# Kernel tuning notes

Hardware: AMD Instinct MI355X
Metric: run time of the kernel (lower is better)

Reference implementation:

```python
import jax, jax.numpy as jnp
import numpy as np
import math

BATCH = 8192
INPUT_DIM = 4096
N_FEATURES = 2048
HAD = 4096  # 2**ceil(log2(max(input_dim, n_features)))
SCALE = math.sqrt(2.0 / N_FEATURES)
INV_SQRT_HAD = 1.0 / math.sqrt(HAD)


def fwht(x):
    """Fast Walsh-Hadamard transform, exact replica of the torch butterfly.
    x: [B, HAD] -> [B, HAD], scaled by 1/sqrt(HAD)."""
    B = x.shape[0]
    h = 1
    while h < HAD:  # log2(HAD) iterations, fixed at trace time
        x = x.reshape(B, -1, h, 2)
        x = jnp.concatenate([x[..., 0] + x[..., 1], x[..., 0] - x[..., 1]], axis=-1)
        x = x.reshape(B, -1)
        h *= 2
    return x * INV_SQRT_HAD


def setup_inputs() -> dict:
    key = jax.random.key(0)
    kx, k1, k2, k3, kp, kb = jax.random.split(key, 6)
    x = jax.random.normal(kx, (BATCH, INPUT_DIM), dtype=jnp.float32)
    D1 = jnp.sign(jax.random.normal(k1, (HAD,), dtype=jnp.float32))
    D2 = jnp.sign(jax.random.normal(k2, (HAD,), dtype=jnp.float32))
    D3 = jnp.sign(jax.random.normal(k3, (HAD,), dtype=jnp.float32))
    perm = jax.random.permutation(kp, HAD)
    bias = jax.random.uniform(kb, (N_FEATURES,), dtype=jnp.float32) * (2.0 * math.pi)
    return {"x": x, "D1": D1, "D2": D2, "D3": D3, "bias": bias, "perm": perm}


def reference(x, D1, D2, D3, bias, perm):
    # pad to hadamard_dim if needed (no-op here since INPUT_DIM == HAD)
    if x.shape[1] < HAD:
        x = jnp.pad(x, ((0, 0), (0, HAD - x.shape[1])))
    x = x * D1
    x = fwht(x)
    x = x * D2
    x = fwht(x)
    x = x * D3
    x = x[:, perm]          # random permutation of columns
    x = x[:, :N_FEATURES]   # keep first n_features columns
    return SCALE * jnp.cos(x + bias)
```

## Files before the change

### kernel.cpp

```cpp
#include <hip/hip_runtime.h>

#define HADN 4096
#define NFEAT 2048
#define INV2PI 0.15915494309189535f

typedef float floatx4 __attribute__((ext_vector_type(4)));
typedef const __attribute__((address_space(1))) void* gas_cptr;
typedef __attribute__((address_space(3))) void* las_ptr;

__device__ __forceinline__ void gload_lds16(const float* g, float* l) {
  __builtin_amdgcn_global_load_lds(
      (gas_cptr)(unsigned long long)g,
      (las_ptr)(unsigned)(unsigned long long)l, 16, 0, 0);
}

__device__ __host__ __forceinline__ int pi_map(int q) {
  return  (((q >> 3) & 1))
        | (((q >> 11) & 1) << 1)
        | (((q >> 7) & 1) << 2)
        | (((q >> 1) & 1) << 3)
        | (((q >> 5) & 1) << 4)
        | (((q >> 9) & 1) << 5)
        | (((q >> 0) & 1) << 6)
        | (((q >> 2) & 1) << 7)
        | (((q >> 4) & 1) << 8)
        | (((q >> 6) & 1) << 9)
        | (((q >> 8) & 1) << 10)
        | (((q >> 10) & 1) << 11);
}

__device__ __host__ __forceinline__ int pi_inv_map(int p) {
  return  (((p >> 6) & 1))
        | (((p >> 3) & 1) << 1)
        | (((p >> 7) & 1) << 2)
        | (((p >> 0) & 1) << 3)
        | (((p >> 8) & 1) << 4)
        | (((p >> 4) & 1) << 5)
        | (((p >> 9) & 1) << 6)
        | (((p >> 2) & 1) << 7)
        | (((p >> 10) & 1) << 8)
        | (((p >> 5) & 1) << 9)
        | (((p >> 11) & 1) << 10)
        | (((p >> 1) & 1) << 11);
}

__device__ __forceinline__ int swz(int p) {
  return p ^ ((((p >> 6) ^ (p >> 9)) & 7) << 2);
}

template <int BIT>
__device__ __forceinline__ void bfly(float* r) {
#pragma unroll
  for (int e = 0; e < 16; ++e) {
    if ((e & BIT) == 0) {
      const int f = e | BIT;
      const float a = r[e], b = r[f];
      r[e] = a + b;
      r[f] = a - b;
    }
  }
}

template <int CTRL>
__device__ __forceinline__ void dpp_bfly(float* r, bool upper) {
  const unsigned sm = upper ? 0x80000000u : 0u;
#pragma unroll
  for (int e = 0; e < 16; ++e) {
    const int pv = __builtin_amdgcn_update_dpp(
        0, __float_as_int(r[e]), CTRL, 0xF, 0xF, true);
    r[e] = __int_as_float(pv) + __int_as_float(__float_as_int(r[e]) ^ sm);
  }
}

__global__ __launch_bounds__(256) void srf_setup(
    const float* __restrict__ D1, const float* __restrict__ D2,
    const float* __restrict__ D3, const int* __restrict__ perm,
    const float* __restrict__ bias,
    unsigned* __restrict__ D1sgn, unsigned* __restrict__ D2sgn,
    float* __restrict__ dgc, int* __restrict__ gidx,
    float* __restrict__ bzc) {
  const int i = blockIdx.x * 256 + threadIdx.x;
  const bool b1 = (__float_as_uint(D1[i]) >> 31) != 0;
  const bool b2 = (__float_as_uint(D2[pi_inv_map(i)]) >> 31) != 0;
  const unsigned long long m1 = __ballot(b1);
  const unsigned long long m2 = __ballot(b2);
  const int lane = i & 63;
  if ((lane & 31) == 0) {
    D1sgn[i >> 5] = (unsigned)(m1 >> (lane & 32));
    D2sgn[i >> 5] = (unsigned)(m2 >> (lane & 32));
  }
  if (i < NFEAT) {
    const int j = perm[i];
    gidx[i] = swz(pi_map(pi_map(j)));
    dgc[i] = 0.0625f * INV2PI * D3[j];
    bzc[i] = INV2PI * bias[i];
  }
}

__global__ __launch_bounds__(512) void srf_main(
    const float* __restrict__ x,
    const unsigned* __restrict__ D1sgn, const unsigned* __restrict__ D2sgn,
    const float* __restrict__ dgc, const int* __restrict__ gidx,
    const float* __restrict__ bzc, float* __restrict__ out) {
  __shared__ float lds[2][HADN];
  const int tid = threadIdx.x;
  const int rr = tid >> 8;
  const int t256 = tid & 255;
  const long row = (long)blockIdx.x * 2;
  const int l = tid & 63;
  const int w = (tid >> 6) & 3;
  const int base = (((l >> 2) & 1) << 2) | ((l & 1) << 5) | (((l >> 3) & 1) << 6)
                 | (((l >> 4) & 1) << 7) | (((l >> 1) & 1) << 8)
                 | (((l >> 5) & 1) << 9) | (w << 10);

  const float* xr = x + (row + rr) * HADN;
#pragma unroll
  for (int k = 0; k < 4; ++k) {
    const int p = (k * 256 + t256) * 4;
    gload_lds16(xr + swz(p), &lds[rr][p]);
  }

  const unsigned sw1 = D1sgn[base >> 5] >> (base & 4);
  const unsigned sw2 = D2sgn[base >> 5] >> (base & 4);
  const int o = tid * 4;
  const int4   gi = *(const int4*)(gidx + o);
  const float4 dg = *(const float4*)(dgc + o);
  const float4 bz = *(const float4*)(bzc + o);
  __syncthreads();

  float r[16];
  float* L = &lds[rr][0];
#pragma unroll
  for (int g = 0; g < 4; ++g) {
    const int p = base | ((g & 1) << 3) | (((g >> 1) & 1) << 4);
    const float4 v = *(const float4*)(L + swz(p));
    r[g * 4 + 0] = v.x; r[g * 4 + 1] = v.y; r[g * 4 + 2] = v.z; r[g * 4 + 3] = v.w;
  }
#pragma unroll
  for (int e = 0; e < 16; ++e) {
    const int pos = (e & 3) | ((e & 12) << 1);
    r[e] = __int_as_float(__float_as_int(r[e]) ^ ((sw1 >> pos) << 31));
  }
  bfly<2>(r); bfly<4>(r); bfly<8>(r);
  dpp_bfly<0xB1>(r, (l & 1) != 0);
#pragma unroll
  for (int e = 0; e < 16; ++e) {
    const int pos = (e & 3) | ((e & 12) << 1);
    r[e] = __int_as_float(__float_as_int(r[e]) ^ ((sw2 >> pos) << 31));
  }
  bfly<1>(r); bfly<4>(r); bfly<8>(r);
  dpp_bfly<0x4E>(r, (l & 2) != 0);

#pragma unroll
  for (int g = 0; g < 4; ++g) {
    const int p = base | ((g & 1) << 3) | (((g >> 1) & 1) << 4);
    const float4 v = make_float4(r[g * 4 + 0], r[g * 4 + 1], r[g * 4 + 2], r[g * 4 + 3]);
    *(float4*)(L + swz(p)) = v;
  }
  __syncthreads();

  float* op = out + row * NFEAT;
  floatx4 res0;
  res0.x = 0.03125f * __builtin_amdgcn_cosf(fmaf(lds[0][gi.x], dg.x, bz.x));
  res0.y = 0.03125f * __builtin_amdgcn_cosf(fmaf(lds[0][gi.y], dg.y, bz.y));
  res0.z = 0.03125f * __builtin_amdgcn_cosf(fmaf(lds[0][gi.z], dg.z, bz.z));
  res0.w = 0.03125f * __builtin_amdgcn_cosf(fmaf(lds[0][gi.w], dg.w, bz.w));
  __builtin_nontemporal_store(res0, (floatx4*)(op + o));
  floatx4 res1;
  res1.x = 0.03125f * __builtin_amdgcn_cosf(fmaf(lds[1][gi.x], dg.x, bz.x));
  res1.y = 0.03125f * __builtin_amdgcn_cosf(fmaf(lds[1][gi.y], dg.y, bz.y));
  res1.z = 0.03125f * __builtin_amdgcn_cosf(fmaf(lds[1][gi.z], dg.z, bz.z));
  res1.w = 0.03125f * __builtin_amdgcn_cosf(fmaf(lds[1][gi.w], dg.w, bz.w));
  __builtin_nontemporal_store(res1, (floatx4*)(op + NFEAT + o));
}

extern "C" void kernel_launch(void* const* d_in, const int* in_sizes, int n_in,
                              void* d_out, int out_size, void* d_ws, size_t ws_size,
                              hipStream_t stream) {
  const float* x    = (const float*)d_in[0];
  const float* D1   = (const float*)d_in[1];
  const float* D2   = (const float*)d_in[2];
  const float* D3   = (const float*)d_in[3];
  const float* bias = (const float*)d_in[4];
  const int*   perm = (const int*)d_in[5];
  float* out = (float*)d_out;

  unsigned* D1sgn = (unsigned*)d_ws;
  unsigned* D2sgn = D1sgn + 128;
  float*    dgc   = (float*)(D2sgn + 128);
  int*      gidx  = (int*)(dgc + NFEAT);
  float*    bzc   = (float*)(gidx + NFEAT);

  srf_setup<<<16, 256, 0, stream>>>(D1, D2, D3, perm, bias,
                                    D1sgn, D2sgn, dgc, gidx, bzc);
  srf_main<<<4096, 512, 0, stream>>>(x, D1sgn, D2sgn, dgc, gidx, bzc, out);
}
```

Baseline: 40.01 us.

## Fuse setup into main kernel and process multiple row pairs per block

Removes the separate setup kernel. Each block now builds the D1/D2 sign bitmasks in LDS and computes the gather indices and scales itself. Each block also loops over four row pairs, which amortises that setup and cuts the grid to 1024 blocks. The next rows are loaded only after the current outputs are written, with no overlap between the two. That leaves the loop serialised, and fewer blocks can reduce latency hiding.

Result: slower. 44.66 us (+11.6%).

```diff
diff --git a/kernel.cpp b/kernel.cpp
--- a/kernel.cpp
+++ b/kernel.cpp
@@ -2,6 +2,8 @@
 
 #define HADN 4096
 #define NFEAT 2048
+#define ROWS_PER_IT 2
+#define ITERS 4
 #define INV2PI 0.15915494309189535f
 
 typedef float floatx4 __attribute__((ext_vector_type(4)));
@@ -14,7 +16,7 @@
       (las_ptr)(unsigned)(unsigned long long)l, 16, 0, 0);
 }
 
-__device__ __host__ __forceinline__ int pi_map(int q) {
+__device__ __forceinline__ int pi_map(int q) {
   return  (((q >> 3) & 1))
         | (((q >> 11) & 1) << 1)
         | (((q >> 7) & 1) << 2)
@@ -29,7 +31,7 @@
         | (((q >> 10) & 1) << 11);
 }
 
-__device__ __host__ __forceinline__ int pi_inv_map(int p) {
+__device__ __forceinline__ int pi_inv_map(int p) {
   return  (((p >> 6) & 1))
         | (((p >> 3) & 1) << 1)
         | (((p >> 7) & 1) << 2)
@@ -72,106 +74,122 @@
   }
 }
 
-__global__ __launch_bounds__(256) void srf_setup(
-    const float* __restrict__ D1, const float* __restrict__ D2,
-    const float* __restrict__ D3, const int* __restrict__ perm,
-    const float* __restrict__ bias,
-    unsigned* __restrict__ D1sgn, unsigned* __restrict__ D2sgn,
-    float* __restrict__ dgc, int* __restrict__ gidx,
-    float* __restrict__ bzc) {
-  const int i = blockIdx.x * 256 + threadIdx.x;
-  const bool b1 = (__float_as_uint(D1[i]) >> 31) != 0;
-  const bool b2 = (__float_as_uint(D2[pi_inv_map(i)]) >> 31) != 0;
-  const unsigned long long m1 = __ballot(b1);
-  const unsigned long long m2 = __ballot(b2);
-  const int lane = i & 63;
-  if ((lane & 31) == 0) {
-    D1sgn[i >> 5] = (unsigned)(m1 >> (lane & 32));
-    D2sgn[i >> 5] = (unsigned)(m2 >> (lane & 32));
-  }
-  if (i < NFEAT) {
-    const int j = perm[i];
-    gidx[i] = swz(pi_map(pi_map(j)));
-    dgc[i] = 0.0625f * INV2PI * D3[j];
-    bzc[i] = INV2PI * bias[i];
-  }
-}
-
-__global__ __launch_bounds__(512) void srf_main(
-    const float* __restrict__ x,
-    const unsigned* __restrict__ D1sgn, const unsigned* __restrict__ D2sgn,
-    const float* __restrict__ dgc, const int* __restrict__ gidx,
-    const float* __restrict__ bzc, float* __restrict__ out) {
-  __shared__ float lds[2][HADN];
+__global__ __launch_bounds__(512) void srf_all(
+    const float* __restrict__ x, const float* __restrict__ D1,
+    const float* __restrict__ D2, const float* __restrict__ D3,
+    const int* __restrict__ perm, const float* __restrict__ bias,
+    float* __restrict__ out) {
+  __shared__ float lds[ROWS_PER_IT][HADN];
+  __shared__ unsigned sgn[2][HADN / 32];
   const int tid = threadIdx.x;
   const int rr = tid >> 8;
   const int t256 = tid & 255;
-  const long row = (long)blockIdx.x * 2;
   const int l = tid & 63;
   const int w = (tid >> 6) & 3;
+  const int lane = tid & 63;
+  const long row0 = (long)blockIdx.x * (ROWS_PER_IT * ITERS);
   const int base = (((l >> 2) & 1) << 2) | ((l & 1) << 5) | (((l >> 3) & 1) << 6)
                  | (((l >> 4) & 1) << 7) | (((l >> 1) & 1) << 8)
                  | (((l >> 5) & 1) << 9) | (w << 10);
 
-  const float* xr = x + (row + rr) * HADN;
-#pragma unroll
-  for (int k = 0; k < 4; ++k) {
-    const int p = (k * 256 + t256) * 4;
-    gload_lds16(xr + swz(p), &lds[rr][p]);
-  }
-
-  const unsigned sw1 = D1sgn[base >> 5] >> (base & 4);
-  const unsigned sw2 = D2sgn[base >> 5] >> (base & 4);
+  {
+    const float* xr = x + (row0 + rr) * HADN;
+#pragma unroll
+    for (int k = 0; k < 4; ++k) {
+      const int p = (k * 256 + t256) * 4;
+      gload_lds16(xr + swz(p), &lds[rr][p]);
+    }
+  }
+
+#pragma unroll
+  for (int j = 0; j < 8; ++j) {
+    const int idx = j * 512 + tid;
+    const bool b1 = (__float_as_uint(D1[idx]) >> 31) != 0;
+    const bool b2 = (__float_as_uint(D2[pi_inv_map(idx)]) >> 31) != 0;
+    const unsigned long long m1 = __ballot(b1);
+    const unsigned long long m2 = __ballot(b2);
+    if ((lane & 31) == 0) {
+      sgn[0][idx >> 5] = (unsigned)(m1 >> (lane & 32));
+      sgn[1][idx >> 5] = (unsigned)(m2 >> (lane & 32));
+    }
+  }
+
   const int o = tid * 4;
-  const int4   gi = *(const int4*)(gidx + o);
-  const float4 dg = *(const float4*)(dgc + o);
-  const float4 bz = *(const float4*)(bzc + o);
+  const int4 pj = *(const int4*)(perm + o);
+  int4 gi;
+  gi.x = swz(pi_map(pi_map(pj.x)));
+  gi.y = swz(pi_map(pi_map(pj.y)));
+  gi.z = swz(pi_map(pi_map(pj.z)));
+  gi.w = swz(pi_map(pi_map(pj.w)));
+  float4 dg;
+  dg.x = 0.0625f * INV2PI * D3[pj.x];
+  dg.y = 0.0625f * INV2PI * D3[pj.y];
+  dg.z = 0.0625f * INV2PI * D3[pj.z];
+  dg.w = 0.0625f * INV2PI * D3[pj.w];
+  float4 bz = *(const float4*)(bias + o);
+  bz.x *= INV2PI; bz.y *= INV2PI; bz.z *= INV2PI; bz.w *= INV2PI;
+
   __syncthreads();
-
-  float r[16];
-  float* L = &lds[rr][0];
-#pragma unroll
-  for (int g = 0; g < 4; ++g) {
-    const int p = base | ((g & 1) << 3) | (((g >> 1) & 1) << 4);
-    const float4 v = *(const float4*)(L + swz(p));
-    r[g * 4 + 0] = v.x; r[g * 4 + 1] = v.y; r[g * 4 + 2] = v.z; r[g * 4 + 3] = v.w;
-  }
-#pragma unroll
-  for (int e = 0; e < 16; ++e) {
-    const int pos = (e & 3) | ((e & 12) << 1);
-    r[e] = __int_as_float(__float_as_int(r[e]) ^ ((sw1 >> pos) << 31));
-  }
-  bfly<2>(r); bfly<4>(r); bfly<8>(r);
-  dpp_bfly<0xB1>(r, (l & 1) != 0);
-#pragma unroll
-  for (int e = 0; e < 16; ++e) {
-    const int pos = (e & 3) | ((e & 12) << 1);
-    r[e] = __int_as_float(__float_as_int(r[e]) ^ ((sw2 >> pos) << 31));
-  }
-  bfly<1>(r); bfly<4>(r); bfly<8>(r);
-  dpp_bfly<0x4E>(r, (l & 2) != 0);
-
-#pragma unroll
-  for (int g = 0; g < 4; ++g) {
-    const int p = base | ((g & 1) << 3) | (((g >> 1) & 1) << 4);
-    const float4 v = make_float4(r[g * 4 + 0], r[g * 4 + 1], r[g * 4 + 2], r[g * 4 + 3]);
-    *(float4*)(L + swz(p)) = v;
-  }
-  __syncthreads();
-
-  float* op = out + row * NFEAT;
-  floatx4 res0;
-  res0.x = 0.03125f * __builtin_amdgcn_cosf(fmaf(lds[0][gi.x], dg.x, bz.x));
-  res0.y = 0.03125f * __builtin_amdgcn_cosf(fmaf(lds[0][gi.y], dg.y, bz.y));
-  res0.z = 0.03125f * __builtin_amdgcn_cosf(fmaf(lds[0][gi.z], dg.z, bz.z));
-  res0.w = 0.03125f * __builtin_amdgcn_cosf(fmaf(lds[0][gi.w], dg.w, bz.w));
-  __builtin_nontemporal_store(res0, (floatx4*)(op + o));
-  floatx4 res1;
-  res1.x = 0.03125f * __builtin_amdgcn_cosf(fmaf(lds[1][gi.x], dg.x, bz.x));
-  res1.y = 0.03125f * __builtin_amdgcn_cosf(fmaf(lds[1][gi.y], dg.y, bz.y));
-  res1.z = 0.03125f * __builtin_amdgcn_cosf(fmaf(lds[1][gi.z], dg.z, bz.z));
-  res1.w = 0.03125f * __builtin_amdgcn_cosf(fmaf(lds[1][gi.w], dg.w, bz.w));
-  __builtin_nontemporal_store(res1, (floatx4*)(op + NFEAT + o));
+  const unsigned sw1 = sgn[0][base >> 5] >> (base & 4);
+  const unsigned sw2 = sgn[1][base >> 5] >> (base & 4);
+
+  for (int it = 0; it < ITERS; ++it) {
+    float r[16];
+    float* L = &lds[rr][0];
+#pragma unroll
+    for (int g = 0; g < 4; ++g) {
+      const int p = base | ((g & 1) << 3) | (((g >> 1) & 1) << 4);
+      const float4 v = *(const float4*)(L + swz(p));
+      r[g * 4 + 0] = v.x; r[g * 4 + 1] = v.y; r[g * 4 + 2] = v.z; r[g * 4 + 3] = v.w;
+    }
+#pragma unroll
+    for (int e = 0; e < 16; ++e) {
+      const int pos = (e & 3) | ((e & 12) << 1);
+      r[e] = __int_as_float(__float_as_int(r[e]) ^ ((sw1 >> pos) << 31));
+    }
+    bfly<2>(r); bfly<4>(r); bfly<8>(r);
+    dpp_bfly<0xB1>(r, (l & 1) != 0);
+#pragma unroll
+    for (int e = 0; e < 16; ++e) {
+      const int pos = (e & 3) | ((e & 12) << 1);
+      r[e] = __int_as_float(__float_as_int(r[e]) ^ ((sw2 >> pos) << 31));
+    }
+    bfly<1>(r); bfly<4>(r); bfly<8>(r);
+    dpp_bfly<0x4E>(r, (l & 2) != 0);
+#pragma unroll
+    for (int g = 0; g < 4; ++g) {
+      const int p = base | ((g & 1) << 3) | (((g >> 1) & 1) << 4);
+      const float4 v = make_float4(r[g * 4 + 0], r[g * 4 + 1], r[g * 4 + 2], r[g * 4 + 3]);
+      *(float4*)(L + swz(p)) = v;
+    }
+    __syncthreads();
+
+    const long row = row0 + (long)it * ROWS_PER_IT;
+    float* op = out + row * NFEAT;
+    floatx4 res0;
+    res0.x = 0.03125f * __builtin_amdgcn_cosf(fmaf(lds[0][gi.x], dg.x, bz.x));
+    res0.y = 0.03125f * __builtin_amdgcn_cosf(fmaf(lds[0][gi.y], dg.y, bz.y));
+    res0.z = 0.03125f * __builtin_amdgcn_cosf(fmaf(lds[0][gi.z], dg.z, bz.z));
+    res0.w = 0.03125f * __builtin_amdgcn_cosf(fmaf(lds[0][gi.w], dg.w, bz.w));
+    __builtin_nontemporal_store(res0, (floatx4*)(op + o));
+    floatx4 res1;
+    res1.x = 0.03125f * __builtin_amdgcn_cosf(fmaf(lds[1][gi.x], dg.x, bz.x));
+    res1.y = 0.03125f * __builtin_amdgcn_cosf(fmaf(lds[1][gi.y], dg.y, bz.y));
+    res1.z = 0.03125f * __builtin_amdgcn_cosf(fmaf(lds[1][gi.z], dg.z, bz.z));
+    res1.w = 0.03125f * __builtin_amdgcn_cosf(fmaf(lds[1][gi.w], dg.w, bz.w));
+    __builtin_nontemporal_store(res1, (floatx4*)(op + NFEAT + o));
+
+    if (it < ITERS - 1) {
+      __syncthreads();
+      const float* xn = x + (row + ROWS_PER_IT + rr) * HADN;
+#pragma unroll
+      for (int k = 0; k < 4; ++k) {
+        const int p = (k * 256 + t256) * 4;
+        gload_lds16(xn + swz(p), &lds[rr][p]);
+      }
+      __syncthreads();
+    }
+  }
 }
 
 extern "C" void kernel_launch(void* const* d_in, const int* in_sizes, int n_in,
@@ -185,13 +203,6 @@
   const int*   perm = (const int*)d_in[5];
   float* out = (float*)d_out;
 
-  unsigned* D1sgn = (unsigned*)d_ws;
-  unsigned* D2sgn = D1sgn + 128;
-  float*    dgc   = (float*)(D2sgn + 128);
-  int*      gidx  = (int*)(dgc + NFEAT);
-  float*    bzc   = (float*)(gidx + NFEAT);
-
-  srf_setup<<<16, 256, 0, stream>>>(D1, D2, D3, perm, bias,
-                                    D1sgn, D2sgn, dgc, gidx, bzc);
-  srf_main<<<4096, 512, 0, stream>>>(x, D1sgn, D2sgn, dgc, gidx, bzc, out);
-}
+  srf_all<<<8192 / (ROWS_PER_IT * ITERS), 512, 0, stream>>>(
+      x, D1, D2, D3, perm, bias, out);
+}
```
